# Optimization experiments

Measured on AMD Instinct MI355X. Metric: run time of the kernel, lower is better.

Reference implementation:

```python
import jax, jax.numpy as jnp
import numpy as np

B, TE, TD, HE, HD = 8, 256, 256, 512, 512


def setup_inputs() -> dict:
    key = jax.random.key(0)
    k1, k2, k3, k4, k5 = jax.random.split(key, 5)
    return {
        "encoder_out_seq": jax.random.normal(k1, (B, TE, HE), dtype=jnp.float32),
        "decoder_out_seq": jax.random.normal(k2, (B, TD, HD), dtype=jnp.float32),
        "W_a": jax.random.normal(k3, (HE, HE), dtype=jnp.float32) * 0.05,
        "U_a": jax.random.normal(k4, (HD, HE), dtype=jnp.float32) * 0.05,
        "V_a": jax.random.normal(k5, (HE, 1), dtype=jnp.float32) * 0.05,
    }


def reference(encoder_out_seq, decoder_out_seq, W_a, U_a, V_a):
    # Bahdanau additive attention, vectorized over all decoder timesteps.
    # Hoist encoder projection (the K.rnn version recomputed this each step).
    Ws = jnp.einsum('bth,hk->btk', encoder_out_seq, W_a)      # [B, Te, He]
    Uh = jnp.einsum('bdh,hk->bdk', decoder_out_seq, U_a)     # [B, Td, He]
    # tanh(S.Wa + hj.Ua) -> score via V_a, softmax over encoder axis Te
    scores = jnp.einsum('bdtk,k->bdt',
                        jnp.tanh(Ws[:, None, :, :] + Uh[:, :, None, :]),
                        V_a[:, 0])                            # [B, Td, Te]
    e = jax.nn.softmax(scores, axis=-1)                       # energies
    c = jnp.einsum('bdt,bth->bdh', e, encoder_out_seq)        # contexts [B, Td, He]
    return c, e
```

## Files before the change

kernel.cpp:

```cpp
#include <hip/hip_runtime.h>
#include <hip/hip_bf16.h>


#define BB  8
#define TEE 256
#define TDD 256
#define HH  512
#define C2LOG2E 2.8853900817779268f
#define SLAB ((size_t)BB * TDD * TEE)
#define NKS 8

typedef __attribute__((ext_vector_type(8))) short  short8;
typedef __attribute__((ext_vector_type(4))) float  floatx4;

__device__ __forceinline__ unsigned short f2bf(float f) {
  __hip_bfloat16 h = __float2bfloat16(f);
  return __builtin_bit_cast(unsigned short, h);
}

__global__ __launch_bounds__(256) void proj_all(
    const float* __restrict__ enc, const float* __restrict__ dec,
    const float* __restrict__ Wa,  const float* __restrict__ Ua,
    float* __restrict__ EW, float* __restrict__ EU,
    unsigned short* __restrict__ encT)
{
  __shared__ float tile[64][65];
  const int bid = blockIdx.x;

  if (bid < 512) {
    const int side = bid >> 8;
    const int lb = bid & 255;
    const float* X = side ? dec : enc;
    const float* W = side ? Ua  : Wa;
    float*       Y = side ? EU  : EW;
    const int lane = threadIdx.x & 63, w = threadIdx.x >> 6;
    const int m0 = (lb >> 3) * 64 + w * 16;
    const int n0 = (lb & 7) * 64;
    const int r15 = lane & 15, g = lane >> 4;

    floatx4 acc[4] = {{0.f,0.f,0.f,0.f},{0.f,0.f,0.f,0.f},
                      {0.f,0.f,0.f,0.f},{0.f,0.f,0.f,0.f}};
    const float* ap = X + (size_t)(m0 + r15) * HH + g * 8;

    for (int k0 = 0; k0 < HH; k0 += 32) {
      float4 a0 = *(const float4*)(ap + k0);
      float4 a1 = *(const float4*)(ap + k0 + 4);
      short8 a;
      a[0]=(short)f2bf(a0.x*C2LOG2E); a[1]=(short)f2bf(a0.y*C2LOG2E);
      a[2]=(short)f2bf(a0.z*C2LOG2E); a[3]=(short)f2bf(a0.w*C2LOG2E);
      a[4]=(short)f2bf(a1.x*C2LOG2E); a[5]=(short)f2bf(a1.y*C2LOG2E);
      a[6]=(short)f2bf(a1.z*C2LOG2E); a[7]=(short)f2bf(a1.w*C2LOG2E);
      const float* wrow = W + (size_t)(k0 + g * 8) * HH + n0 + r15;
      #pragma unroll
      for (int nt = 0; nt < 4; ++nt) {
        short8 bv;
        #pragma unroll
        for (int j = 0; j < 8; ++j) bv[j] = (short)f2bf(wrow[(size_t)j * HH + nt * 16]);
        acc[nt] = __builtin_amdgcn_mfma_f32_16x16x32_bf16(a, bv, acc[nt], 0, 0, 0);
      }
    }
    #pragma unroll
    for (int nt = 0; nt < 4; ++nt) {
      float* yp = Y + (size_t)(m0 + g * 4) * HH + n0 + nt * 16 + r15;
      #pragma unroll
      for (int r = 0; r < 4; ++r) {
        float v = fminf(fmaxf(acc[nt][r], -15.f), 15.f);
        yp[(size_t)r * HH] = __builtin_amdgcn_exp2f(v);
      }
    }
  } else {
    const int idx = bid - 512;
    const int b  = idx >> 5;
    const int h0 = ((idx >> 2) & 7) * 64;
    const int t0 = (idx & 3) * 64;
    const int c = threadIdx.x & 63, r4 = threadIdx.x >> 6;
    #pragma unroll
    for (int i = 0; i < 16; ++i) {
      int tr = i * 4 + r4;
      tile[tr][c] = enc[((size_t)b * TEE + t0 + tr) * HH + h0 + c];
    }
    __syncthreads();
    #pragma unroll
    for (int i = 0; i < 16; ++i) {
      int hr = i * 4 + r4;
      encT[((size_t)b * HH + h0 + hr) * TEE + t0 + c] = f2bf(tile[c][hr]);
    }
  }
}

__global__ __launch_bounds__(256) void score_rt(
    const float* __restrict__ EW, const float* __restrict__ EU,
    const float* __restrict__ Va, float* __restrict__ Apart)
{
  __shared__ float swT[2][32][68];
  __shared__ float suT[2][32][68];

  const int b  = blockIdx.z;
  const int ks = blockIdx.x >> 2;
  const int t0 = (blockIdx.x & 3) * 64;
  const int d0 = blockIdx.y * 64;
  const int kbase = ks * 64;
  const int tid = threadIdx.x;
  const int tx = tid & 15, ty = tid >> 4;
  const int sr = tid >> 2, fq = tid & 3;
  const int kq = fq * 4;

  const float* wsrc = EW + ((size_t)(b * TEE) + t0 + sr) * HH + kbase + kq;
  const float* usrc = EU + ((size_t)(b * TDD) + d0 + sr) * HH + kbase + kq;

  float acc[4][4] = {};

#define STAGE(BUF_, W0_, W1_, U0_, U1_) {                         \
    swT[BUF_][kq + 0][sr] = W0_.x; swT[BUF_][kq + 1][sr] = W0_.y; \
    swT[BUF_][kq + 2][sr] = W0_.z; swT[BUF_][kq + 3][sr] = W0_.w; \
    swT[BUF_][kq +16][sr] = W1_.x; swT[BUF_][kq +17][sr] = W1_.y; \
    swT[BUF_][kq +18][sr] = W1_.z; swT[BUF_][kq +19][sr] = W1_.w; \
    suT[BUF_][kq + 0][sr] = U0_.x; suT[BUF_][kq + 1][sr] = U0_.y; \
    suT[BUF_][kq + 2][sr] = U0_.z; suT[BUF_][kq + 3][sr] = U0_.w; \
    suT[BUF_][kq +16][sr] = U1_.x; suT[BUF_][kq +17][sr] = U1_.y; \
    suT[BUF_][kq +18][sr] = U1_.z; suT[BUF_][kq +19][sr] = U1_.w; }

  {
    float4 w0 = *(const float4*)(wsrc);
    float4 w1 = *(const float4*)(wsrc + 16);
    float4 u0 = *(const float4*)(usrc);
    float4 u1 = *(const float4*)(usrc + 16);
    STAGE(0, w0, w1, u0, u1)
  }

  for (int ch = 0; ch < 2; ++ch) {
    float4 nw0, nw1, nu0, nu1;
    const bool more = (ch == 0);
    if (more) {
      nw0 = *(const float4*)(wsrc + 32);
      nw1 = *(const float4*)(wsrc + 48);
      nu0 = *(const float4*)(usrc + 32);
      nu1 = *(const float4*)(usrc + 48);
    }
    __syncthreads();

    const float* vb = Va + kbase + ch * 32;

    #pragma unroll 2
    for (int kk = 0; kk < 32; kk += 4) {
      floatx4 wA = *(const floatx4*)&swT[ch][kk    ][tx * 4];
      floatx4 wB = *(const floatx4*)&swT[ch][kk + 1][tx * 4];
      floatx4 wC = *(const floatx4*)&swT[ch][kk + 2][tx * 4];
      floatx4 wD = *(const floatx4*)&swT[ch][kk + 3][tx * 4];
      floatx4 uA = *(const floatx4*)&suT[ch][kk    ][ty * 4];
      floatx4 uB = *(const floatx4*)&suT[ch][kk + 1][ty * 4];
      floatx4 uC = *(const floatx4*)&suT[ch][kk + 2][ty * 4];
      floatx4 uD = *(const floatx4*)&suT[ch][kk + 3][ty * 4];
      float4 vv = *(const float4*)(vb + kk);
      #pragma unroll
      for (int j = 0; j < 4; ++j) {
        float u1 = uA[j], u2 = uB[j], u3 = uC[j], u4 = uD[j];
        #pragma unroll
        for (int i = 0; i < 4; ++i) {
          float A1 = fmaf(wA[i], u1, 1.0f);
          float B1 = fmaf(wB[i], u2, 1.0f);
          float C1 = fmaf(wC[i], u3, 1.0f);
          float D1 = fmaf(wD[i], u4, 1.0f);
          float dab = A1 * B1;
          float nab = fmaf(vv.x, B1, vv.y * A1);
          float dcd = C1 * D1;
          float ncd = fmaf(vv.z, D1, vv.w * C1);
          float den = dab * dcd;
          float num = fmaf(nab, dcd, ncd * dab);
          acc[j][i] = fmaf(num, __builtin_amdgcn_rcpf(den), acc[j][i]);
        }
      }
    }

    if (more) STAGE(1, nw0, nw1, nu0, nu1)
  }
#undef STAGE

  float* Ap = Apart + (size_t)ks * SLAB;
  #pragma unroll
  for (int j = 0; j < 4; ++j) {
    const int d = d0 + ty * 4 + j;
    floatx4 o = {acc[j][0], acc[j][1], acc[j][2], acc[j][3]};
    *(floatx4*)(Ap + ((size_t)(b * TDD) + d) * TEE + t0 + tx * 4) = o;
  }
}

__global__ __launch_bounds__(256) void ctx_fused(
    const float* __restrict__ Apart, const unsigned short* __restrict__ encT,
    float* __restrict__ c, float* __restrict__ e_out)
{
  __shared__ unsigned short pe[16][264];

  const int b  = blockIdx.z;
  const int d0 = blockIdx.x * 16;
  const int h0 = blockIdx.y * 128;
  const int lane = threadIdx.x & 63, w = threadIdx.x >> 6;

  {
    const int row  = w * 4 + (lane >> 4);
    const int col0 = (lane & 15) * 16;
    const size_t base = ((size_t)(b * TDD) + d0 + row) * TEE + col0;
    float x[16];
    #pragma unroll
    for (int q = 0; q < 4; ++q) {
      floatx4 v = *(const floatx4*)(Apart + base + q * 4);
      x[4*q] = v[0]; x[4*q+1] = v[1]; x[4*q+2] = v[2]; x[4*q+3] = v[3];
    }
    #pragma unroll
    for (int s = 1; s < NKS; ++s) {
      #pragma unroll
      for (int q = 0; q < 4; ++q) {
        floatx4 v = *(const floatx4*)(Apart + (size_t)s * SLAB + base + q * 4);
        x[4*q] += v[0]; x[4*q+1] += v[1]; x[4*q+2] += v[2]; x[4*q+3] += v[3];
      }
    }
    float m = x[0];
    #pragma unroll
    for (int j = 1; j < 16; ++j) m = fminf(m, x[j]);
    #pragma unroll
    for (int off = 8; off; off >>= 1) m = fminf(m, __shfl_xor(m, off));
    float p[16], s = 0.f;
    #pragma unroll
    for (int j = 0; j < 16; ++j) {
      p[j] = __builtin_amdgcn_exp2f(C2LOG2E * (m - x[j]));
      s += p[j];
    }
    #pragma unroll
    for (int off = 8; off; off >>= 1) s += __shfl_xor(s, off);
    float r = __builtin_amdgcn_rcpf(s);

    #pragma unroll
    for (int j = 0; j < 16; j += 2) {
      float v0 = p[j] * r, v1 = p[j+1] * r;
      *(ushort2*)&pe[row][col0 + j] = make_ushort2(f2bf(v0), f2bf(v1));
    }
    if (blockIdx.y == 0) {
      float* er = e_out + ((size_t)(b * TDD) + d0 + row) * TEE + col0;
      #pragma unroll
      for (int j = 0; j < 16; ++j) er[j] = p[j] * r;
    }
  }
  __syncthreads();

  const int r15 = lane & 15, g = lane >> 4;
  const int hw = h0 + w * 32;
  floatx4 acc0 = {0.f,0.f,0.f,0.f}, acc1 = {0.f,0.f,0.f,0.f};
  const unsigned short* bp0 = encT + ((size_t)b * HH + hw + r15) * TEE + g * 8;

  for (int k0 = 0; k0 < TEE; k0 += 32) {
    short8 a = *(const short8*)(&pe[r15][k0 + g * 8]);
    short8 bv0 = *(const short8*)(bp0 + k0);
    short8 bv1 = *(const short8*)(bp0 + (size_t)16 * TEE + k0);
    acc0 = __builtin_amdgcn_mfma_f32_16x16x32_bf16(a, bv0, acc0, 0, 0, 0);
    acc1 = __builtin_amdgcn_mfma_f32_16x16x32_bf16(a, bv1, acc1, 0, 0, 0);
  }
  floatx4 aall[2] = {acc0, acc1};
  #pragma unroll
  for (int nt = 0; nt < 2; ++nt) {
    float* cp = c + ((size_t)(b * TDD) + d0 + g * 4) * HH + hw + nt * 16 + r15;
    #pragma unroll
    for (int r = 0; r < 4; ++r) cp[(size_t)r * HH] = aall[nt][r];
  }
}

extern "C" void kernel_launch(void* const* d_in, const int* in_sizes, int n_in,
                              void* d_out, int out_size, void* d_ws, size_t ws_size,
                              hipStream_t stream) {
  const float* enc = (const float*)d_in[0];
  const float* dec = (const float*)d_in[1];
  const float* Wa  = (const float*)d_in[2];
  const float* Ua  = (const float*)d_in[3];
  const float* Va  = (const float*)d_in[4];

  float* c_out = (float*)d_out;
  float* e_out = c_out + (size_t)BB * TDD * HH;

  unsigned short* encT = (unsigned short*)d_ws;
  float* EW    = (float*)(encT + (size_t)BB * HH * TEE);
  float* EU    = EW + (size_t)BB * TEE * HH;
  float* Apart = EU + (size_t)BB * TDD * HH;

  proj_all  <<<768,              256, 0, stream>>>(enc, dec, Wa, Ua, EW, EU, encT);
  score_rt  <<<dim3(32, 4, 8),   256, 0, stream>>>(EW, EU, Va, Apart);
  ctx_fused <<<dim3(16, 4, 8),   256, 0, stream>>>(Apart, encT, c_out, e_out);
}
```

Baseline: 60.93 us.

## Fuse three kernels into one cooperative kernel with grid-wide syncs

Merges the projection, score and context kernels into a single cooperative-launch kernel of 512 blocks, separated by grid.sync barriers. The transpose work moves onto blocks 256-511 after their projection tile, and the score stage loops over two tiles per block. This removes two kernel launch gaps, but adds grid-barrier cost and relies on all 512 blocks being co-resident, which the launch-bounds hint of two blocks per CU is meant to allow.

```diff
diff --git a/kernel.cpp b/kernel.cpp
--- a/kernel.cpp
+++ b/kernel.cpp
@@ -1,5 +1,8 @@
 #include <hip/hip_runtime.h>
 #include <hip/hip_bf16.h>
+#include <hip/hip_cooperative_groups.h>
+
+namespace cg = cooperative_groups;
 
 
 #define BB  8
@@ -18,22 +21,30 @@
   return __builtin_bit_cast(unsigned short, h);
 }
 
-__global__ __launch_bounds__(256) void proj_all(
+struct SmemScore { float swT[2][32][68]; float suT[2][32][68]; };
+struct SmemProj  { float tile[64][65]; };
+struct SmemCtx   { unsigned short pe[16][264]; };
+
+__global__ void __launch_bounds__(256, 2) mega_kernel(
     const float* __restrict__ enc, const float* __restrict__ dec,
     const float* __restrict__ Wa,  const float* __restrict__ Ua,
+    const float* __restrict__ Va,
     float* __restrict__ EW, float* __restrict__ EU,
-    unsigned short* __restrict__ encT)
+    float* __restrict__ Apart, unsigned short* __restrict__ encT,
+    float* __restrict__ c_out, float* __restrict__ e_out)
 {
-  __shared__ float tile[64][65];
+  cg::grid_group grid = cg::this_grid();
+  __shared__ __align__(16) char smem[sizeof(SmemScore)];
   const int bid = blockIdx.x;
-
-  if (bid < 512) {
+  const int tid = threadIdx.x;
+
+  {
     const int side = bid >> 8;
     const int lb = bid & 255;
     const float* X = side ? dec : enc;
     const float* W = side ? Ua  : Wa;
     float*       Y = side ? EU  : EW;
-    const int lane = threadIdx.x & 63, w = threadIdx.x >> 6;
+    const int lane = tid & 63, w = tid >> 6;
     const int m0 = (lb >> 3) * 64 + w * 16;
     const int n0 = (lb & 7) * 64;
     const int r15 = lane & 15, g = lane >> 4;
@@ -68,198 +79,198 @@
         yp[(size_t)r * HH] = __builtin_amdgcn_exp2f(v);
       }
     }
-  } else {
-    const int idx = bid - 512;
-    const int b  = idx >> 5;
-    const int h0 = ((idx >> 2) & 7) * 64;
-    const int t0 = (idx & 3) * 64;
-    const int c = threadIdx.x & 63, r4 = threadIdx.x >> 6;
+
+    if (bid >= 256) {
+      SmemProj* sp = (SmemProj*)smem;
+      const int idx = bid - 256;
+      const int b  = idx >> 5;
+      const int h0 = ((idx >> 2) & 7) * 64;
+      const int t0 = (idx & 3) * 64;
+      const int c = tid & 63, r4 = tid >> 6;
+      #pragma unroll
+      for (int i = 0; i < 16; ++i) {
+        int tr = i * 4 + r4;
+        sp->tile[tr][c] = enc[((size_t)b * TEE + t0 + tr) * HH + h0 + c];
+      }
+      __syncthreads();
+      #pragma unroll
+      for (int i = 0; i < 16; ++i) {
+        int hr = i * 4 + r4;
+        encT[((size_t)b * HH + h0 + hr) * TEE + t0 + c] = f2bf(sp->tile[c][hr]);
+      }
+    }
+  }
+
+  grid.sync();
+
+  {
+    SmemScore* sm = (SmemScore*)smem;
+    for (int T = bid; T < 1024; T += 512) {
+      const int x  = T & 31, y = (T >> 5) & 3, b = T >> 7;
+      const int ks = x >> 2;
+      const int t0 = (x & 3) * 64;
+      const int d0 = y * 64;
+      const int kbase = ks * 64;
+      const int tx = tid & 15, ty = tid >> 4;
+      const int sr = tid >> 2, fq = tid & 3;
+      const int kq = fq * 4;
+
+      const float* wsrc = EW + ((size_t)(b * TEE) + t0 + sr) * HH + kbase + kq;
+      const float* usrc = EU + ((size_t)(b * TDD) + d0 + sr) * HH + kbase + kq;
+
+      float acc[4][4] = {};
+
+#define STAGE(BUF_, W0_, W1_, U0_, U1_) {                                 \
+    sm->swT[BUF_][kq + 0][sr] = W0_.x; sm->swT[BUF_][kq + 1][sr] = W0_.y; \
+    sm->swT[BUF_][kq + 2][sr] = W0_.z; sm->swT[BUF_][kq + 3][sr] = W0_.w; \
+    sm->swT[BUF_][kq +16][sr] = W1_.x; sm->swT[BUF_][kq +17][sr] = W1_.y; \
+    sm->swT[BUF_][kq +18][sr] = W1_.z; sm->swT[BUF_][kq +19][sr] = W1_.w; \
+    sm->suT[BUF_][kq + 0][sr] = U0_.x; sm->suT[BUF_][kq + 1][sr] = U0_.y; \
+    sm->suT[BUF_][kq + 2][sr] = U0_.z; sm->suT[BUF_][kq + 3][sr] = U0_.w; \
+    sm->suT[BUF_][kq +16][sr] = U1_.x; sm->suT[BUF_][kq +17][sr] = U1_.y; \
+    sm->suT[BUF_][kq +18][sr] = U1_.z; sm->suT[BUF_][kq +19][sr] = U1_.w; }
+
+      {
+        float4 w0 = *(const float4*)(wsrc);
+        float4 w1 = *(const float4*)(wsrc + 16);
+        float4 u0 = *(const float4*)(usrc);
+        float4 u1 = *(const float4*)(usrc + 16);
+        STAGE(0, w0, w1, u0, u1)
+      }
+
+      for (int ch = 0; ch < 2; ++ch) {
+        float4 nw0, nw1, nu0, nu1;
+        const bool more = (ch == 0);
+        if (more) {
+          nw0 = *(const float4*)(wsrc + 32);
+          nw1 = *(const float4*)(wsrc + 48);
+          nu0 = *(const float4*)(usrc + 32);
+          nu1 = *(const float4*)(usrc + 48);
+        }
+        __syncthreads();
+
+        const float* vb = Va + kbase + ch * 32;
+
+        #pragma unroll 2
+        for (int kk = 0; kk < 32; kk += 4) {
+          floatx4 wA = *(const floatx4*)&sm->swT[ch][kk    ][tx * 4];
+          floatx4 wB = *(const floatx4*)&sm->swT[ch][kk + 1][tx * 4];
+          floatx4 wC = *(const floatx4*)&sm->swT[ch][kk + 2][tx * 4];
+          floatx4 wD = *(const floatx4*)&sm->swT[ch][kk + 3][tx * 4];
+          floatx4 uA = *(const floatx4*)&sm->suT[ch][kk    ][ty * 4];
+          floatx4 uB = *(const floatx4*)&sm->suT[ch][kk + 1][ty * 4];
+          floatx4 uC = *(const floatx4*)&sm->suT[ch][kk + 2][ty * 4];
+          floatx4 uD = *(const floatx4*)&sm->suT[ch][kk + 3][ty * 4];
+          float4 vv = *(const float4*)(vb + kk);
+          #pragma unroll
+          for (int j = 0; j < 4; ++j) {
+            float u1 = uA[j], u2 = uB[j], u3 = uC[j], u4 = uD[j];
+            #pragma unroll
+            for (int i = 0; i < 4; ++i) {
+              float A1 = fmaf(wA[i], u1, 1.0f);
+              float B1 = fmaf(wB[i], u2, 1.0f);
+              float C1 = fmaf(wC[i], u3, 1.0f);
+              float D1 = fmaf(wD[i], u4, 1.0f);
+              float dab = A1 * B1;
+              float nab = fmaf(vv.x, B1, vv.y * A1);
+              float dcd = C1 * D1;
+              float ncd = fmaf(vv.z, D1, vv.w * C1);
+              float den = dab * dcd;
+              float num = fmaf(nab, dcd, ncd * dab);
+              acc[j][i] = fmaf(num, __builtin_amdgcn_rcpf(den), acc[j][i]);
+            }
+          }
+        }
+
+        if (more) STAGE(1, nw0, nw1, nu0, nu1)
+      }
+#undef STAGE
+
+      float* Ap = Apart + (size_t)ks * SLAB;
+      #pragma unroll
+      for (int j = 0; j < 4; ++j) {
+        const int d = d0 + ty * 4 + j;
+        floatx4 o = {acc[j][0], acc[j][1], acc[j][2], acc[j][3]};
+        *(floatx4*)(Ap + ((size_t)(b * TDD) + d) * TEE + t0 + tx * 4) = o;
+      }
+      __syncthreads();
+    }
+  }
+
+  grid.sync();
+
+  {
+    SmemCtx* sc = (SmemCtx*)smem;
+    const int cx = bid & 15, cyq = (bid >> 4) & 3, b = bid >> 6;
+    const int d0 = cx * 16;
+    const int h0 = cyq * 128;
+    const int lane = tid & 63, w = tid >> 6;
+
+    {
+      const int row  = w * 4 + (lane >> 4);
+      const int col0 = (lane & 15) * 16;
+      const size_t base = ((size_t)(b * TDD) + d0 + row) * TEE + col0;
+      float x[16];
+      #pragma unroll
+      for (int q = 0; q < 4; ++q) {
+        floatx4 v = *(const floatx4*)(Apart + base + q * 4);
+        x[4*q] = v[0]; x[4*q+1] = v[1]; x[4*q+2] = v[2]; x[4*q+3] = v[3];
+      }
+      #pragma unroll
+      for (int s = 1; s < NKS; ++s) {
+        #pragma unroll
+        for (int q = 0; q < 4; ++q) {
+          floatx4 v = *(const floatx4*)(Apart + (size_t)s * SLAB + base + q * 4);
+          x[4*q] += v[0]; x[4*q+1] += v[1]; x[4*q+2] += v[2]; x[4*q+3] += v[3];
+        }
+      }
+      float m = x[0];
+      #pragma unroll
+      for (int j = 1; j < 16; ++j) m = fminf(m, x[j]);
+      #pragma unroll
+      for (int off = 8; off; off >>= 1) m = fminf(m, __shfl_xor(m, off));
+      float p[16], s = 0.f;
+      #pragma unroll
+      for (int j = 0; j < 16; ++j) {
+        p[j] = __builtin_amdgcn_exp2f(C2LOG2E * (m - x[j]));
+        s += p[j];
+      }
+      #pragma unroll
+      for (int off = 8; off; off >>= 1) s += __shfl_xor(s, off);
+      float r = __builtin_amdgcn_rcpf(s);
+
+      #pragma unroll
+      for (int j = 0; j < 16; j += 2) {
+        float v0 = p[j] * r, v1 = p[j+1] * r;
+        *(ushort2*)&sc->pe[row][col0 + j] = make_ushort2(f2bf(v0), f2bf(v1));
+      }
+      if (cyq == 0) {
+        float* er = e_out + ((size_t)(b * TDD) + d0 + row) * TEE + col0;
+        #pragma unroll
+        for (int j = 0; j < 16; ++j) er[j] = p[j] * r;
+      }
+    }
+    __syncthreads();
+
+    const int r15 = lane & 15, g = lane >> 4;
+    const int hw = h0 + w * 32;
+    floatx4 acc0 = {0.f,0.f,0.f,0.f}, acc1 = {0.f,0.f,0.f,0.f};
+    const unsigned short* bp0 = encT + ((size_t)b * HH + hw + r15) * TEE + g * 8;
+
+    for (int k0 = 0; k0 < TEE; k0 += 32) {
+      short8 a = *(const short8*)(&sc->pe[r15][k0 + g * 8]);
+      short8 bv0 = *(const short8*)(bp0 + k0);
+      short8 bv1 = *(const short8*)(bp0 + (size_t)16 * TEE + k0);
+      acc0 = __builtin_amdgcn_mfma_f32_16x16x32_bf16(a, bv0, acc0, 0, 0, 0);
+      acc1 = __builtin_amdgcn_mfma_f32_16x16x32_bf16(a, bv1, acc1, 0, 0, 0);
+    }
+    floatx4 aall[2] = {acc0, acc1};
     #pragma unroll
-    for (int i = 0; i < 16; ++i) {
-      int tr = i * 4 + r4;
-      tile[tr][c] = enc[((size_t)b * TEE + t0 + tr) * HH + h0 + c];
-    }
-    __syncthreads();
-    #pragma unroll
-    for (int i = 0; i < 16; ++i) {
-      int hr = i * 4 + r4;
-      encT[((size_t)b * HH + h0 + hr) * TEE + t0 + c] = f2bf(tile[c][hr]);
-    }
-  }
-}
-
-__global__ __launch_bounds__(256) void score_rt(
-    const float* __restrict__ EW, const float* __restrict__ EU,
-    const float* __restrict__ Va, float* __restrict__ Apart)
-{
-  __shared__ float swT[2][32][68];
-  __shared__ float suT[2][32][68];
-
-  const int b  = blockIdx.z;
-  const int ks = blockIdx.x >> 2;
-  const int t0 = (blockIdx.x & 3) * 64;
-  const int d0 = blockIdx.y * 64;
-  const int kbase = ks * 64;
-  const int tid = threadIdx.x;
-  const int tx = tid & 15, ty = tid >> 4;
-  const int sr = tid >> 2, fq = tid & 3;
-  const int kq = fq * 4;
-
-  const float* wsrc = EW + ((size_t)(b * TEE) + t0 + sr) * HH + kbase + kq;
-  const float* usrc = EU + ((size_t)(b * TDD) + d0 + sr) * HH + kbase + kq;
-
-  float acc[4][4] = {};
-
-#define STAGE(BUF_, W0_, W1_, U0_, U1_) {                         \
-    swT[BUF_][kq + 0][sr] = W0_.x; swT[BUF_][kq + 1][sr] = W0_.y; \
-    swT[BUF_][kq + 2][sr] = W0_.z; swT[BUF_][kq + 3][sr] = W0_.w; \
-    swT[BUF_][kq +16][sr] = W1_.x; swT[BUF_][kq +17][sr] = W1_.y; \
-    swT[BUF_][kq +18][sr] = W1_.z; swT[BUF_][kq +19][sr] = W1_.w; \
-    suT[BUF_][kq + 0][sr] = U0_.x; suT[BUF_][kq + 1][sr] = U0_.y; \
-    suT[BUF_][kq + 2][sr] = U0_.z; suT[BUF_][kq + 3][sr] = U0_.w; \
-    suT[BUF_][kq +16][sr] = U1_.x; suT[BUF_][kq +17][sr] = U1_.y; \
-    suT[BUF_][kq +18][sr] = U1_.z; suT[BUF_][kq +19][sr] = U1_.w; }
-
-  {
-    float4 w0 = *(const float4*)(wsrc);
-    float4 w1 = *(const float4*)(wsrc + 16);
-    float4 u0 = *(const float4*)(usrc);
-    float4 u1 = *(const float4*)(usrc + 16);
-    STAGE(0, w0, w1, u0, u1)
-  }
-
-  for (int ch = 0; ch < 2; ++ch) {
-    float4 nw0, nw1, nu0, nu1;
-    const bool more = (ch == 0);
-    if (more) {
-      nw0 = *(const float4*)(wsrc + 32);
-      nw1 = *(const float4*)(wsrc + 48);
-      nu0 = *(const float4*)(usrc + 32);
-      nu1 = *(const float4*)(usrc + 48);
-    }
-    __syncthreads();
-
-    const float* vb = Va + kbase + ch * 32;
-
-    #pragma unroll 2
-    for (int kk = 0; kk < 32; kk += 4) {
-      floatx4 wA = *(const floatx4*)&swT[ch][kk    ][tx * 4];
-      floatx4 wB = *(const floatx4*)&swT[ch][kk + 1][tx * 4];
-      floatx4 wC = *(const floatx4*)&swT[ch][kk + 2][tx * 4];
-      floatx4 wD = *(const floatx4*)&swT[ch][kk + 3][tx * 4];
-      floatx4 uA = *(const floatx4*)&suT[ch][kk    ][ty * 4];
-      floatx4 uB = *(const floatx4*)&suT[ch][kk + 1][ty * 4];
-      floatx4 uC = *(const floatx4*)&suT[ch][kk + 2][ty * 4];
-      floatx4 uD = *(const floatx4*)&suT[ch][kk + 3][ty * 4];
-      float4 vv = *(const float4*)(vb + kk);
-      #pragma unroll
-      for (int j = 0; j < 4; ++j) {
-        float u1 = uA[j], u2 = uB[j], u3 = uC[j], u4 = uD[j];
-        #pragma unroll
-        for (int i = 0; i < 4; ++i) {
-          float A1 = fmaf(wA[i], u1, 1.0f);
-          float B1 = fmaf(wB[i], u2, 1.0f);
-          float C1 = fmaf(wC[i], u3, 1.0f);
-          float D1 = fmaf(wD[i], u4, 1.0f);
-          float dab = A1 * B1;
-          float nab = fmaf(vv.x, B1, vv.y * A1);
-          float dcd = C1 * D1;
-          float ncd = fmaf(vv.z, D1, vv.w * C1);
-          float den = dab * dcd;
-          float num = fmaf(nab, dcd, ncd * dab);
-          acc[j][i] = fmaf(num, __builtin_amdgcn_rcpf(den), acc[j][i]);
-        }
-      }
-    }
-
-    if (more) STAGE(1, nw0, nw1, nu0, nu1)
-  }
-#undef STAGE
-
-  float* Ap = Apart + (size_t)ks * SLAB;
-  #pragma unroll
-  for (int j = 0; j < 4; ++j) {
-    const int d = d0 + ty * 4 + j;
-    floatx4 o = {acc[j][0], acc[j][1], acc[j][2], acc[j][3]};
-    *(floatx4*)(Ap + ((size_t)(b * TDD) + d) * TEE + t0 + tx * 4) = o;
-  }
-}
-
-__global__ __launch_bounds__(256) void ctx_fused(
-    const float* __restrict__ Apart, const unsigned short* __restrict__ encT,
-    float* __restrict__ c, float* __restrict__ e_out)
-{
-  __shared__ unsigned short pe[16][264];
-
-  const int b  = blockIdx.z;
-  const int d0 = blockIdx.x * 16;
-  const int h0 = blockIdx.y * 128;
-  const int lane = threadIdx.x & 63, w = threadIdx.x >> 6;
-
-  {
-    const int row  = w * 4 + (lane >> 4);
-    const int col0 = (lane & 15) * 16;
-    const size_t base = ((size_t)(b * TDD) + d0 + row) * TEE + col0;
-    float x[16];
-    #pragma unroll
-    for (int q = 0; q < 4; ++q) {
-      floatx4 v = *(const floatx4*)(Apart + base + q * 4);
-      x[4*q] = v[0]; x[4*q+1] = v[1]; x[4*q+2] = v[2]; x[4*q+3] = v[3];
-    }
-    #pragma unroll
-    for (int s = 1; s < NKS; ++s) {
-      #pragma unroll
-      for (int q = 0; q < 4; ++q) {
-        floatx4 v = *(const floatx4*)(Apart + (size_t)s * SLAB + base + q * 4);
-        x[4*q] += v[0]; x[4*q+1] += v[1]; x[4*q+2] += v[2]; x[4*q+3] += v[3];
-      }
-    }
-    float m = x[0];
-    #pragma unroll
-    for (int j = 1; j < 16; ++j) m = fminf(m, x[j]);
-    #pragma unroll
-    for (int off = 8; off; off >>= 1) m = fminf(m, __shfl_xor(m, off));
-    float p[16], s = 0.f;
-    #pragma unroll
-    for (int j = 0; j < 16; ++j) {
-      p[j] = __builtin_amdgcn_exp2f(C2LOG2E * (m - x[j]));
-      s += p[j];
-    }
-    #pragma unroll
-    for (int off = 8; off; off >>= 1) s += __shfl_xor(s, off);
-    float r = __builtin_amdgcn_rcpf(s);
-
-    #pragma unroll
-    for (int j = 0; j < 16; j += 2) {
-      float v0 = p[j] * r, v1 = p[j+1] * r;
-      *(ushort2*)&pe[row][col0 + j] = make_ushort2(f2bf(v0), f2bf(v1));
-    }
-    if (blockIdx.y == 0) {
-      float* er = e_out + ((size_t)(b * TDD) + d0 + row) * TEE + col0;
-      #pragma unroll
-      for (int j = 0; j < 16; ++j) er[j] = p[j] * r;
-    }
-  }
-  __syncthreads();
-
-  const int r15 = lane & 15, g = lane >> 4;
-  const int hw = h0 + w * 32;
-  floatx4 acc0 = {0.f,0.f,0.f,0.f}, acc1 = {0.f,0.f,0.f,0.f};
-  const unsigned short* bp0 = encT + ((size_t)b * HH + hw + r15) * TEE + g * 8;
-
-  for (int k0 = 0; k0 < TEE; k0 += 32) {
-    short8 a = *(const short8*)(&pe[r15][k0 + g * 8]);
-    short8 bv0 = *(const short8*)(bp0 + k0);
-    short8 bv1 = *(const short8*)(bp0 + (size_t)16 * TEE + k0);
-    acc0 = __builtin_amdgcn_mfma_f32_16x16x32_bf16(a, bv0, acc0, 0, 0, 0);
-    acc1 = __builtin_amdgcn_mfma_f32_16x16x32_bf16(a, bv1, acc1, 0, 0, 0);
-  }
-  floatx4 aall[2] = {acc0, acc1};
-  #pragma unroll
-  for (int nt = 0; nt < 2; ++nt) {
-    float* cp = c + ((size_t)(b * TDD) + d0 + g * 4) * HH + hw + nt * 16 + r15;
-    #pragma unroll
-    for (int r = 0; r < 4; ++r) cp[(size_t)r * HH] = aall[nt][r];
+    for (int nt = 0; nt < 2; ++nt) {
+      float* cp = c_out + ((size_t)(b * TDD) + d0 + g * 4) * HH + hw + nt * 16 + r15;
+      #pragma unroll
+      for (int r = 0; r < 4; ++r) cp[(size_t)r * HH] = aall[nt][r];
+    }
   }
 }
 
@@ -280,7 +291,9 @@
   float* EU    = EW + (size_t)BB * TEE * HH;
   float* Apart = EU + (size_t)BB * TDD * HH;
 
-  proj_all  <<<768,              256, 0, stream>>>(enc, dec, Wa, Ua, EW, EU, encT);
-  score_rt  <<<dim3(32, 4, 8),   256, 0, stream>>>(EW, EU, Va, Apart);
-  ctx_fused <<<dim3(16, 4, 8),   256, 0, stream>>>(Apart, encT, c_out, e_out);
+  void* kargs[] = { (void*)&enc, (void*)&dec, (void*)&Wa, (void*)&Ua, (void*)&Va,
+                    (void*)&EW, (void*)&EU, (void*)&Apart, (void*)&encT,
+                    (void*)&c_out, (void*)&e_out };
+  hipLaunchCooperativeKernel((const void*)mega_kernel, dim3(512), dim3(256),
+                             kargs, 0, stream);
 }
```

Result: slower. 183.7 us (+201.4%).

## Fuse score, softmax and context into one kernel with k-interleaved EW layout

Applied to the files above, without the earlier changes.

Merges the split-K score kernel and the context kernel into a single fused kernel. Each block handles 8 decoder rows, keeps EU rows in shared memory, and streams EW in a new k4-interleaved layout written by the projection kernel. The 8-slab partial-score buffer and its global round trip go away, along with one launch. In exchange the grid shrinks to 256 blocks of 512 threads, each thread does a long serial k-loop, and the context MFMA wastes half its rows because only 8 decoder rows are active.

```diff
diff --git a/kernel.cpp b/kernel.cpp
--- a/kernel.cpp
+++ b/kernel.cpp
@@ -7,8 +7,6 @@
 #define TDD 256
 #define HH  512
 #define C2LOG2E 2.8853900817779268f
-#define SLAB ((size_t)BB * TDD * TEE)
-#define NKS 8
 
 typedef __attribute__((ext_vector_type(8))) short  short8;
 typedef __attribute__((ext_vector_type(4))) float  floatx4;
@@ -18,23 +16,24 @@
   return __builtin_bit_cast(unsigned short, h);
 }
 
-__global__ __launch_bounds__(256) void proj_all(
+__global__ __launch_bounds__(256) void prep_proj(
     const float* __restrict__ enc, const float* __restrict__ dec,
     const float* __restrict__ Wa,  const float* __restrict__ Ua,
-    float* __restrict__ EW, float* __restrict__ EU,
+    float* __restrict__ EW4, float* __restrict__ EU,
     unsigned short* __restrict__ encT)
 {
-  __shared__ float tile[64][65];
+  __shared__ float tile[64][68];
   const int bid = blockIdx.x;
+  const int tid = threadIdx.x;
 
   if (bid < 512) {
     const int side = bid >> 8;
     const int lb = bid & 255;
     const float* X = side ? dec : enc;
     const float* W = side ? Ua  : Wa;
-    float*       Y = side ? EU  : EW;
-    const int lane = threadIdx.x & 63, w = threadIdx.x >> 6;
-    const int m0 = (lb >> 3) * 64 + w * 16;
+    const int lane = tid & 63, w = tid >> 6;
+    const int m0b = (lb >> 3) * 64;
+    const int m0 = m0b + w * 16;
     const int n0 = (lb & 7) * 64;
     const int r15 = lane & 15, g = lane >> 4;
 
@@ -59,13 +58,36 @@
         acc[nt] = __builtin_amdgcn_mfma_f32_16x16x32_bf16(a, bv, acc[nt], 0, 0, 0);
       }
     }
-    #pragma unroll
-    for (int nt = 0; nt < 4; ++nt) {
-      float* yp = Y + (size_t)(m0 + g * 4) * HH + n0 + nt * 16 + r15;
-      #pragma unroll
-      for (int r = 0; r < 4; ++r) {
-        float v = fminf(fmaxf(acc[nt][r], -15.f), 15.f);
-        yp[(size_t)r * HH] = __builtin_amdgcn_exp2f(v);
+    if (side == 1) {
+      #pragma unroll
+      for (int nt = 0; nt < 4; ++nt) {
+        float* yp = EU + (size_t)(m0 + g * 4) * HH + n0 + nt * 16 + r15;
+        #pragma unroll
+        for (int r = 0; r < 4; ++r) {
+          float v = fminf(fmaxf(acc[nt][r], -15.f), 15.f);
+          yp[(size_t)r * HH] = __builtin_amdgcn_exp2f(v);
+        }
+      }
+    } else {
+      #pragma unroll
+      for (int nt = 0; nt < 4; ++nt) {
+        #pragma unroll
+        for (int r = 0; r < 4; ++r) {
+          float v = fminf(fmaxf(acc[nt][r], -15.f), 15.f);
+          tile[w * 16 + g * 4 + r][nt * 16 + r15] = __builtin_amdgcn_exp2f(v);
+        }
+      }
+      __syncthreads();
+      #pragma unroll
+      for (int i = 0; i < 4; ++i) {
+        const int cell = i * 256 + tid;
+        const int tl  = cell & 63;
+        const int k4l = cell >> 6;
+        const int m   = m0b + tl;
+        const int b   = m >> 8, t = m & 255;
+        const int k4  = (n0 >> 2) + k4l;
+        float4 val = *(const float4*)&tile[tl][k4l * 4];
+        *(float4*)(EW4 + (size_t)b * 131072 + (size_t)k4 * 1024 + t * 4) = val;
       }
     }
   } else {
@@ -73,7 +95,7 @@
     const int b  = idx >> 5;
     const int h0 = ((idx >> 2) & 7) * 64;
     const int t0 = (idx & 3) * 64;
-    const int c = threadIdx.x & 63, r4 = threadIdx.x >> 6;
+    const int c = tid & 63, r4 = tid >> 6;
     #pragma unroll
     for (int i = 0; i < 16; ++i) {
       int tr = i * 4 + r4;
@@ -88,178 +110,112 @@
   }
 }
 
-__global__ __launch_bounds__(256) void score_rt(
-    const float* __restrict__ EW, const float* __restrict__ EU,
-    const float* __restrict__ Va, float* __restrict__ Apart)
+__global__ __launch_bounds__(512, 2) void fused(
+    const float* __restrict__ EW4, const float* __restrict__ EU,
+    const float* __restrict__ Va, const unsigned short* __restrict__ encT,
+    float* __restrict__ c_out, float* __restrict__ e_out)
 {
-  __shared__ float swT[2][32][68];
-  __shared__ float suT[2][32][68];
-
-  const int b  = blockIdx.z;
-  const int ks = blockIdx.x >> 2;
-  const int t0 = (blockIdx.x & 3) * 64;
-  const int d0 = blockIdx.y * 64;
-  const int kbase = ks * 64;
+  __shared__ float euL[8][512];
+  __shared__ float As[8][260];
+  __shared__ unsigned short pe[8][264];
+
+  const int bid = blockIdx.x;
+  const int b  = bid >> 5;
+  const int d0 = (bid & 31) * 8;
   const int tid = threadIdx.x;
-  const int tx = tid & 15, ty = tid >> 4;
-  const int sr = tid >> 2, fq = tid & 3;
-  const int kq = fq * 4;
-
-  const float* wsrc = EW + ((size_t)(b * TEE) + t0 + sr) * HH + kbase + kq;
-  const float* usrc = EU + ((size_t)(b * TDD) + d0 + sr) * HH + kbase + kq;
-
-  float acc[4][4] = {};
-
-#define STAGE(BUF_, W0_, W1_, U0_, U1_) {                         \
-    swT[BUF_][kq + 0][sr] = W0_.x; swT[BUF_][kq + 1][sr] = W0_.y; \
-    swT[BUF_][kq + 2][sr] = W0_.z; swT[BUF_][kq + 3][sr] = W0_.w; \
-    swT[BUF_][kq +16][sr] = W1_.x; swT[BUF_][kq +17][sr] = W1_.y; \
-    swT[BUF_][kq +18][sr] = W1_.z; swT[BUF_][kq +19][sr] = W1_.w; \
-    suT[BUF_][kq + 0][sr] = U0_.x; suT[BUF_][kq + 1][sr] = U0_.y; \
-    suT[BUF_][kq + 2][sr] = U0_.z; suT[BUF_][kq + 3][sr] = U0_.w; \
-    suT[BUF_][kq +16][sr] = U1_.x; suT[BUF_][kq +17][sr] = U1_.y; \
-    suT[BUF_][kq +18][sr] = U1_.z; suT[BUF_][kq +19][sr] = U1_.w; }
+  const int t  = tid & 255;
+  const int kh = tid >> 8;
 
   {
-    float4 w0 = *(const float4*)(wsrc);
-    float4 w1 = *(const float4*)(wsrc + 16);
-    float4 u0 = *(const float4*)(usrc);
-    float4 u1 = *(const float4*)(usrc + 16);
-    STAGE(0, w0, w1, u0, u1)
-  }
-
-  for (int ch = 0; ch < 2; ++ch) {
-    float4 nw0, nw1, nu0, nu1;
-    const bool more = (ch == 0);
-    if (more) {
-      nw0 = *(const float4*)(wsrc + 32);
-      nw1 = *(const float4*)(wsrc + 48);
-      nu0 = *(const float4*)(usrc + 32);
-      nu1 = *(const float4*)(usrc + 48);
-    }
-    __syncthreads();
-
-    const float* vb = Va + kbase + ch * 32;
-
-    #pragma unroll 2
-    for (int kk = 0; kk < 32; kk += 4) {
-      floatx4 wA = *(const floatx4*)&swT[ch][kk    ][tx * 4];
-      floatx4 wB = *(const floatx4*)&swT[ch][kk + 1][tx * 4];
-      floatx4 wC = *(const floatx4*)&swT[ch][kk + 2][tx * 4];
-      floatx4 wD = *(const floatx4*)&swT[ch][kk + 3][tx * 4];
-      floatx4 uA = *(const floatx4*)&suT[ch][kk    ][ty * 4];
-      floatx4 uB = *(const floatx4*)&suT[ch][kk + 1][ty * 4];
-      floatx4 uC = *(const floatx4*)&suT[ch][kk + 2][ty * 4];
-      floatx4 uD = *(const floatx4*)&suT[ch][kk + 3][ty * 4];
-      float4 vv = *(const float4*)(vb + kk);
-      #pragma unroll
-      for (int j = 0; j < 4; ++j) {
-        float u1 = uA[j], u2 = uB[j], u3 = uC[j], u4 = uD[j];
-        #pragma unroll
-        for (int i = 0; i < 4; ++i) {
-          float A1 = fmaf(wA[i], u1, 1.0f);
-          float B1 = fmaf(wB[i], u2, 1.0f);
-          float C1 = fmaf(wC[i], u3, 1.0f);
-          float D1 = fmaf(wD[i], u4, 1.0f);
-          float dab = A1 * B1;
-          float nab = fmaf(vv.x, B1, vv.y * A1);
-          float dcd = C1 * D1;
-          float ncd = fmaf(vv.z, D1, vv.w * C1);
-          float den = dab * dcd;
-          float num = fmaf(nab, dcd, ncd * dab);
-          acc[j][i] = fmaf(num, __builtin_amdgcn_rcpf(den), acc[j][i]);
-        }
-      }
-    }
-
-    if (more) STAGE(1, nw0, nw1, nu0, nu1)
-  }
-#undef STAGE
-
-  float* Ap = Apart + (size_t)ks * SLAB;
-  #pragma unroll
-  for (int j = 0; j < 4; ++j) {
-    const int d = d0 + ty * 4 + j;
-    floatx4 o = {acc[j][0], acc[j][1], acc[j][2], acc[j][3]};
-    *(floatx4*)(Ap + ((size_t)(b * TDD) + d) * TEE + t0 + tx * 4) = o;
-  }
-}
-
-__global__ __launch_bounds__(256) void ctx_fused(
-    const float* __restrict__ Apart, const unsigned short* __restrict__ encT,
-    float* __restrict__ c, float* __restrict__ e_out)
-{
-  __shared__ unsigned short pe[16][264];
-
-  const int b  = blockIdx.z;
-  const int d0 = blockIdx.x * 16;
-  const int h0 = blockIdx.y * 128;
-  const int lane = threadIdx.x & 63, w = threadIdx.x >> 6;
-
+    const int dr = tid >> 6, kk = (tid & 63) * 8;
+    const float* src = EU + ((size_t)(b * TDD) + d0 + dr) * HH + kk;
+    float4 u0 = *(const float4*)(src);
+    float4 u1 = *(const float4*)(src + 4);
+    *(float4*)&euL[dr][kk]     = u0;
+    *(float4*)&euL[dr][kk + 4] = u1;
+  }
+  __syncthreads();
+
+  float acc[8] = {};
+  const float* ewp = EW4 + (size_t)b * 131072 + (size_t)kh * 64 * 1024 + t * 4;
+  const float* vap = Va + kh * 256;
+  const int kb = kh * 256;
+
+  #pragma unroll 2
+  for (int kg = 0; kg < 64; ++kg) {
+    float4 ew = *(const float4*)(ewp + (size_t)kg * 1024);
+    float4 v  = *(const float4*)(vap + kg * 4);
+    #pragma unroll
+    for (int d = 0; d < 8; ++d) {
+      float4 u = *(const float4*)&euL[d][kb + kg * 4];
+      float A1 = fmaf(ew.x, u.x, 1.0f);
+      float B1 = fmaf(ew.y, u.y, 1.0f);
+      float C1 = fmaf(ew.z, u.z, 1.0f);
+      float D1 = fmaf(ew.w, u.w, 1.0f);
+      float dab = A1 * B1;
+      float nab = fmaf(v.x, B1, v.y * A1);
+      float dcd = C1 * D1;
+      float ncd = fmaf(v.z, D1, v.w * C1);
+      float den = dab * dcd;
+      float num = fmaf(nab, dcd, ncd * dab);
+      acc[d] = fmaf(num, __builtin_amdgcn_rcpf(den), acc[d]);
+    }
+  }
+
+  if (kh == 0) {
+    #pragma unroll
+    for (int d = 0; d < 8; ++d) As[d][t] = acc[d];
+  }
+  __syncthreads();
+  if (kh == 1) {
+    #pragma unroll
+    for (int d = 0; d < 8; ++d) As[d][t] += acc[d];
+  }
+  __syncthreads();
+
+  const int w = tid >> 6, lane = tid & 63;
   {
-    const int row  = w * 4 + (lane >> 4);
-    const int col0 = (lane & 15) * 16;
-    const size_t base = ((size_t)(b * TDD) + d0 + row) * TEE + col0;
-    float x[16];
-    #pragma unroll
-    for (int q = 0; q < 4; ++q) {
-      floatx4 v = *(const floatx4*)(Apart + base + q * 4);
-      x[4*q] = v[0]; x[4*q+1] = v[1]; x[4*q+2] = v[2]; x[4*q+3] = v[3];
-    }
-    #pragma unroll
-    for (int s = 1; s < NKS; ++s) {
-      #pragma unroll
-      for (int q = 0; q < 4; ++q) {
-        floatx4 v = *(const floatx4*)(Apart + (size_t)s * SLAB + base + q * 4);
-        x[4*q] += v[0]; x[4*q+1] += v[1]; x[4*q+2] += v[2]; x[4*q+3] += v[3];
-      }
-    }
-    float m = x[0];
-    #pragma unroll
-    for (int j = 1; j < 16; ++j) m = fminf(m, x[j]);
-    #pragma unroll
-    for (int off = 8; off; off >>= 1) m = fminf(m, __shfl_xor(m, off));
-    float p[16], s = 0.f;
-    #pragma unroll
-    for (int j = 0; j < 16; ++j) {
-      p[j] = __builtin_amdgcn_exp2f(C2LOG2E * (m - x[j]));
-      s += p[j];
-    }
-    #pragma unroll
-    for (int off = 8; off; off >>= 1) s += __shfl_xor(s, off);
+    float4 x = *(const float4*)&As[w][lane * 4];
+    float m = fminf(fminf(x.x, x.y), fminf(x.z, x.w));
+    #pragma unroll
+    for (int off = 32; off; off >>= 1) m = fminf(m, __shfl_xor(m, off));
+    float p0 = __builtin_amdgcn_exp2f(C2LOG2E * (m - x.x));
+    float p1 = __builtin_amdgcn_exp2f(C2LOG2E * (m - x.y));
+    float p2 = __builtin_amdgcn_exp2f(C2LOG2E * (m - x.z));
+    float p3 = __builtin_amdgcn_exp2f(C2LOG2E * (m - x.w));
+    float s = (p0 + p1) + (p2 + p3);
+    #pragma unroll
+    for (int off = 32; off; off >>= 1) s += __shfl_xor(s, off);
     float r = __builtin_amdgcn_rcpf(s);
-
-    #pragma unroll
-    for (int j = 0; j < 16; j += 2) {
-      float v0 = p[j] * r, v1 = p[j+1] * r;
-      *(ushort2*)&pe[row][col0 + j] = make_ushort2(f2bf(v0), f2bf(v1));
-    }
-    if (blockIdx.y == 0) {
-      float* er = e_out + ((size_t)(b * TDD) + d0 + row) * TEE + col0;
-      #pragma unroll
-      for (int j = 0; j < 16; ++j) er[j] = p[j] * r;
-    }
+    float4 ev = {p0 * r, p1 * r, p2 * r, p3 * r};
+    *(float4*)(e_out + ((size_t)(b * TDD) + d0 + w) * TEE + lane * 4) = ev;
+    *(ushort2*)&pe[w][lane * 4]     = make_ushort2(f2bf(ev.x), f2bf(ev.y));
+    *(ushort2*)&pe[w][lane * 4 + 2] = make_ushort2(f2bf(ev.z), f2bf(ev.w));
   }
   __syncthreads();
 
   const int r15 = lane & 15, g = lane >> 4;
-  const int hw = h0 + w * 32;
-  floatx4 acc0 = {0.f,0.f,0.f,0.f}, acc1 = {0.f,0.f,0.f,0.f};
+  const int hw = w * 64;
+  floatx4 ca[4] = {{0.f,0.f,0.f,0.f},{0.f,0.f,0.f,0.f},
+                   {0.f,0.f,0.f,0.f},{0.f,0.f,0.f,0.f}};
   const unsigned short* bp0 = encT + ((size_t)b * HH + hw + r15) * TEE + g * 8;
 
   for (int k0 = 0; k0 < TEE; k0 += 32) {
-    short8 a = *(const short8*)(&pe[r15][k0 + g * 8]);
-    short8 bv0 = *(const short8*)(bp0 + k0);
-    short8 bv1 = *(const short8*)(bp0 + (size_t)16 * TEE + k0);
-    acc0 = __builtin_amdgcn_mfma_f32_16x16x32_bf16(a, bv0, acc0, 0, 0, 0);
-    acc1 = __builtin_amdgcn_mfma_f32_16x16x32_bf16(a, bv1, acc1, 0, 0, 0);
-  }
-  floatx4 aall[2] = {acc0, acc1};
-  #pragma unroll
-  for (int nt = 0; nt < 2; ++nt) {
-    float* cp = c + ((size_t)(b * TDD) + d0 + g * 4) * HH + hw + nt * 16 + r15;
-    #pragma unroll
-    for (int r = 0; r < 4; ++r) cp[(size_t)r * HH] = aall[nt][r];
+    short8 a = {0,0,0,0,0,0,0,0};
+    if (r15 < 8) a = *(const short8*)&pe[r15][k0 + g * 8];
+    #pragma unroll
+    for (int nt = 0; nt < 4; ++nt) {
+      short8 bv = *(const short8*)(bp0 + (size_t)nt * 16 * TEE + k0);
+      ca[nt] = __builtin_amdgcn_mfma_f32_16x16x32_bf16(a, bv, ca[nt], 0, 0, 0);
+    }
+  }
+  if (g < 2) {
+    #pragma unroll
+    for (int nt = 0; nt < 4; ++nt) {
+      float* cp = c_out + ((size_t)(b * TDD) + d0 + g * 4) * HH + hw + nt * 16 + r15;
+      #pragma unroll
+      for (int r = 0; r < 4; ++r) cp[(size_t)r * HH] = ca[nt][r];
+    }
   }
 }
 
@@ -275,12 +231,10 @@
   float* c_out = (float*)d_out;
   float* e_out = c_out + (size_t)BB * TDD * HH;
 
-  unsigned short* encT = (unsigned short*)d_ws;
-  float* EW    = (float*)(encT + (size_t)BB * HH * TEE);
-  float* EU    = EW + (size_t)BB * TEE * HH;
-  float* Apart = EU + (size_t)BB * TDD * HH;
-
-  proj_all  <<<768,              256, 0, stream>>>(enc, dec, Wa, Ua, EW, EU, encT);
-  score_rt  <<<dim3(32, 4, 8),   256, 0, stream>>>(EW, EU, Va, Apart);
-  ctx_fused <<<dim3(16, 4, 8),   256, 0, stream>>>(Apart, encT, c_out, e_out);
-}
+  float* EW4 = (float*)d_ws;
+  float* EU  = EW4 + (size_t)BB * TEE * HH;
+  unsigned short* encT = (unsigned short*)(EU + (size_t)BB * TDD * HH);
+
+  prep_proj<<<768, 256, 0, stream>>>(enc, dec, Wa, Ua, EW4, EU, encT);
+  fused    <<<256, 512, 0, stream>>>(EW4, EU, Va, encT, c_out, e_out);
+}
```

Result: slower. 63.92 us (+4.9%).
